# Performance work log

Measured on AMD Instinct MI355X. Metric: run time of the kernel, lower is better.

The kernel has to match this reference:

```python
import jax, jax.numpy as jnp
import numpy as np

BS, NQ, NC = 64, 3000, 256
FH, FW, TOPK = 100, 100, 1500
INK_INF = jnp.float32(1e20)


def setup_inputs() -> dict:
    key = jax.random.key(0)
    k1, k2, k3 = jax.random.split(key, 3)
    u = jax.random.uniform(k1, (BS, NQ, 4), dtype=jnp.float32)
    # cx,cy in [0.25,0.75], w,h in [0,0.4] -> xyxy strictly inside [0,1]
    cxcy = 0.25 + 0.5 * u[..., :2]
    wh = 0.4 * u[..., 2:]
    output_coord = jnp.concatenate([cxcy, wh], axis=-1)
    output_class = jax.random.uniform(k2, (BS, NQ, NC), dtype=jnp.float32)
    # valid feature extent [valid_h, valid_w] per image (from ~mask cumsum in original)
    valid_feature_size = jax.random.randint(k3, (BS, 2), 50, FH + 1, dtype=jnp.int32)
    rows = jnp.arange(FH)[None, :, None]
    cols = jnp.arange(FW)[None, None, :]
    padding_mask = (rows >= valid_feature_size[:, 0][:, None, None]) | (
        cols >= valid_feature_size[:, 1][:, None, None]
    )  # (BS, FH, FW) bool, True = padded
    return {
        "output_coord": output_coord,
        "output_class": output_class,
        "valid_feature_size": valid_feature_size,
        "padding_mask": padding_mask,
        "feature_h": FH,
        "feature_w": FW,
        "topk": TOPK,
    }


def reference(output_coord, output_class, valid_feature_size, padding_mask,
              feature_h, feature_w, topk):
    bs = output_coord.shape[0]
    # scores = output_class.max(dim=-1); topk box select
    scores = jnp.max(output_class, axis=-1)                      # (bs, nq)
    _, topk_idx = jax.lax.top_k(scores, topk)                    # (bs, k)
    boxes = jnp.take_along_axis(output_coord, topk_idx[..., None], axis=1)  # (bs,k,4) cxcywh
    # box_cxcywh_to_xyxy
    cxcy, wh = boxes[..., :2], boxes[..., 2:]
    xyxy = jnp.concatenate([cxcy - 0.5 * wh, cxcy + 0.5 * wh], axis=-1)  # (bs,k,4)
    # valid_size.repeat(1,2) -> [vh, vw, vh, vw]
    vfs = valid_feature_size.astype(xyxy.dtype)
    scale = jnp.concatenate([vfs, vfs], axis=-1)[:, None, :]     # (bs,1,4)
    rng = jnp.floor(xyxy * scale).astype(jnp.int32)              # (bs,k,4)
    lx, ly, rx, ry = rng[..., 0], rng[..., 1], rng[..., 2], rng[..., 3]
    rows = jnp.arange(feature_h)
    cols = jnp.arange(feature_w)
    # per-box row/col membership; union over boxes via batched GEMM
    R = ((rows[None, None, :] >= ly[..., None]) & (rows[None, None, :] < ry[..., None])).astype(jnp.float32)  # (bs,k,h)
    C = ((cols[None, None, :] >= lx[..., None]) & (cols[None, None, :] < rx[..., None])).astype(jnp.float32)  # (bs,k,w)
    covered = jnp.einsum('bkh,bkw->bhw', R, C) > 0               # (bs,h,w)
    extra_mask = ~covered                                        # True outside every kept box
    # mask = extra_mask | padding_mask; float masked_fill(-INK_INF)
    full = extra_mask.reshape(bs, -1) | padding_mask.reshape(bs, -1)
    attn_mask = jnp.where(full, -INK_INF, jnp.float32(0.0))      # (bs, h*w)
    return attn_mask
```

## Files before the change

kernel.cpp:

```cpp
#include <hip/hip_runtime.h>

#define BS   64
#define NQ   3000
#define NC   256
#define FH   100
#define FW   100
#define TOPK 1500

__global__ __launch_bounds__(256) void scores_kernel(const float4* __restrict__ cls,
                                                     float* __restrict__ scores) {
    const int tid  = threadIdx.x;
    const int lane = tid & 63;
    const int wave = tid >> 6;
    const int row0 = blockIdx.x * 16 + wave * 4;
    const float4* p = cls + (size_t)row0 * (NC / 4) + lane;
    float4 a = p[0], b = p[64], c = p[128], d = p[192];
    float m0 = fmaxf(fmaxf(a.x, a.y), fmaxf(a.z, a.w));
    float m1 = fmaxf(fmaxf(b.x, b.y), fmaxf(b.z, b.w));
    float m2 = fmaxf(fmaxf(c.x, c.y), fmaxf(c.z, c.w));
    float m3 = fmaxf(fmaxf(d.x, d.y), fmaxf(d.z, d.w));
#pragma unroll
    for (int off = 32; off > 0; off >>= 1) {
        m0 = fmaxf(m0, __shfl_xor(m0, off, 64));
        m1 = fmaxf(m1, __shfl_xor(m1, off, 64));
        m2 = fmaxf(m2, __shfl_xor(m2, off, 64));
        m3 = fmaxf(m3, __shfl_xor(m3, off, 64));
    }
    if (lane < 4) {
        float m = (lane == 0) ? m0 : (lane == 1) ? m1 : (lane == 2) ? m2 : m3;
        scores[row0 + lane] = m;
    }
}

#define NTM 512

__global__ __launch_bounds__(NTM) void mask_kernel(const float4* __restrict__ coord,
                                                   const int* __restrict__ vfs,
                                                   const float* __restrict__ scores,
                                                   float* __restrict__ out) {
    __shared__ unsigned su[NQ];
    __shared__ int      hist[8][256];
    __shared__ unsigned cov[FH * 4];
    __shared__ int      eqlist[NQ];
    __shared__ int      wave_sum[4];
    __shared__ int      s_selbin, s_K, s_ecnt;

    const int b    = blockIdx.x;
    const int tid  = threadIdx.x;
    const int wid  = tid >> 6;

    for (int q = tid; q < NQ; q += NTM)
        su[q] = __float_as_uint(scores[b * NQ + q]);
    for (int i = tid; i < FH * 4; i += NTM) cov[i] = 0u;
    if (tid == 0) s_ecnt = 0;

    unsigned prefix = 0, pmask = 0;
    int K = TOPK;
#pragma unroll
    for (int p = 0; p < 4; ++p) {
        const int shift = 24 - 8 * p;
        for (int i = tid; i < 8 * 256; i += NTM) ((int*)hist)[i] = 0;
        __syncthreads();
        for (int q = tid; q < NQ; q += NTM) {
            unsigned u = su[q];
            if ((u & pmask) == prefix)
                atomicAdd(&hist[wid][(u >> shift) & 0xFF], 1);
        }
        __syncthreads();
        int x = 0, hx = 0, bin = 0;
        if (tid < 256) {
            bin = 255 - tid;
            hx = hist[0][bin] + hist[1][bin] + hist[2][bin] + hist[3][bin] +
                 hist[4][bin] + hist[5][bin] + hist[6][bin] + hist[7][bin];
            x = hx;
#pragma unroll
            for (int off = 1; off < 64; off <<= 1) {
                int y = __shfl_up(x, off, 64);
                if ((tid & 63) >= off) x += y;
            }
            if ((tid & 63) == 63) wave_sum[tid >> 6] = x;
        }
        __syncthreads();
        if (tid < 256) {
            int w = tid >> 6;
            for (int j = 0; j < w; ++j) x += wave_sum[j];
            int ge_incl = x;
            int ge_excl = x - hx;
            if (ge_incl >= K && ge_excl < K) {
                s_selbin = bin;
                s_K      = K - ge_excl;
            }
        }
        __syncthreads();
        prefix |= ((unsigned)s_selbin) << shift;
        pmask  |= (0xFFu << shift);
        K = s_K;
        __syncthreads();
    }
    const unsigned v      = prefix;
    const int      e_take = K;

    const float s0 = (float)vfs[2 * b];
    const float s1 = (float)vfs[2 * b + 1];

    for (int q = tid; q < NQ; q += NTM) {
        unsigned u = su[q];
        if (u > v) {
            float4 c4 = coord[(size_t)b * NQ + q];
            float x1 = c4.x - 0.5f * c4.z, y1 = c4.y - 0.5f * c4.w;
            float x2 = c4.x + 0.5f * c4.z, y2 = c4.y + 0.5f * c4.w;
            int lx = (int)floorf(x1 * s0), ly = (int)floorf(y1 * s1);
            int rx = (int)floorf(x2 * s0), ry = (int)floorf(y2 * s1);
            int h0 = ly > 0 ? ly : 0, h1 = ry < FH ? ry : FH;
            int w0 = lx > 0 ? lx : 0, w1 = rx < FW ? rx : FW;
            if (h0 < h1 && w0 < w1) {
                unsigned m[4];
#pragma unroll
                for (int j = 0; j < 4; ++j) {
                    int lo = w0 - 32 * j; lo = lo < 0 ? 0 : lo;
                    int hi = w1 - 32 * j; hi = hi > 32 ? 32 : hi;
                    unsigned mm = 0u;
                    if (hi > lo) {
                        unsigned top = (hi >= 32) ? 0xFFFFFFFFu : ((1u << hi) - 1u);
                        unsigned bot = (lo <= 0) ? 0u : ((1u << lo) - 1u);
                        mm = top & ~bot;
                    }
                    m[j] = mm;
                }
                for (int h = h0; h < h1; ++h) {
#pragma unroll
                    for (int j = 0; j < 4; ++j)
                        if (m[j]) atomicOr(&cov[h * 4 + j], m[j]);
                }
            }
        } else if (u == v) {
            int i = atomicAdd(&s_ecnt, 1);
            eqlist[i] = q;
        }
    }
    __syncthreads();

    const int E = s_ecnt;
    for (int i = tid; i < E; i += NTM) {
        int q = eqlist[i];
        int r = 0;
        for (int j = 0; j < E; ++j) r += (eqlist[j] < q) ? 1 : 0;
        if (r < e_take) {
            float4 c4 = coord[(size_t)b * NQ + q];
            float x1 = c4.x - 0.5f * c4.z, y1 = c4.y - 0.5f * c4.w;
            float x2 = c4.x + 0.5f * c4.z, y2 = c4.y + 0.5f * c4.w;
            int lx = (int)floorf(x1 * s0), ly = (int)floorf(y1 * s1);
            int rx = (int)floorf(x2 * s0), ry = (int)floorf(y2 * s1);
            int h0 = ly > 0 ? ly : 0, h1 = ry < FH ? ry : FH;
            int w0 = lx > 0 ? lx : 0, w1 = rx < FW ? rx : FW;
            if (h0 < h1 && w0 < w1) {
                for (int h = h0; h < h1; ++h) {
#pragma unroll
                    for (int j = 0; j < 4; ++j) {
                        int lo = w0 - 32 * j; lo = lo < 0 ? 0 : lo;
                        int hi = w1 - 32 * j; hi = hi > 32 ? 32 : hi;
                        if (hi > lo) {
                            unsigned top = (hi >= 32) ? 0xFFFFFFFFu : ((1u << hi) - 1u);
                            unsigned bot = (lo <= 0) ? 0u : ((1u << lo) - 1u);
                            atomicOr(&cov[h * 4 + j], top & ~bot);
                        }
                    }
                }
            }
        }
    }
    __syncthreads();

    const int iv0 = vfs[2 * b], iv1 = vfs[2 * b + 1];
    for (int idx = tid; idx < FH * FW; idx += NTM) {
        int h = idx / FW;
        int w = idx - h * FW;
        bool covered = (cov[h * 4 + (w >> 5)] >> (w & 31)) & 1u;
        bool pad = (h >= iv0) || (w >= iv1);
        out[(size_t)b * (FH * FW) + idx] = (covered && !pad) ? 0.0f : -1e20f;
    }
}

extern "C" void kernel_launch(void* const* d_in, const int* in_sizes, int n_in,
                              void* d_out, int out_size, void* d_ws, size_t ws_size,
                              hipStream_t stream) {
    const float4* coord = (const float4*)d_in[0];
    const float*  cls   = (const float*)d_in[1];
    const int*    vfs   = (const int*)d_in[2];
    float* scores = (float*)d_ws;
    float* out    = (float*)d_out;

    const int rows = BS * NQ;
    scores_kernel<<<rows / 16, 256, 0, stream>>>((const float4*)cls, scores);
    mask_kernel<<<BS, NTM, 0, stream>>>(coord, vfs, scores, out);
}
```

Baseline: 316.4 us.

## Fuse score reduction and mask kernels into one cooperative grid-synced kernel

Replaces the two launches (row-max scores, then per-image radix top-k and mask) with a single cooperative kernel. A 512-block grid computes the scores in a grid-stride loop, then a grid barrier lets the first 64 blocks run the mask phase. This removes one kernel launch and the gap between kernels. In exchange, the whole grid is sized for the heavy shared-memory mask phase, the scores pass runs with fewer resident blocks, and the kernel pays for a grid sync. If the cooperative launch fails, it falls back to the two-kernel path.

```diff
diff --git a/kernel.cpp b/kernel.cpp
--- a/kernel.cpp
+++ b/kernel.cpp
@@ -1,4 +1,7 @@
 #include <hip/hip_runtime.h>
+#include <hip/hip_cooperative_groups.h>
+
+namespace cg = cooperative_groups;
 
 #define BS   64
 #define NQ   3000
@@ -6,6 +9,189 @@
 #define FH   100
 #define FW   100
 #define TOPK 1500
+#define NT   512
+#define NBLK 512
+
+__device__ __forceinline__ void mask_phase(int b, int tid,
+                                           const float4* __restrict__ coord,
+                                           const int* __restrict__ vfs,
+                                           const float* __restrict__ scores,
+                                           float* __restrict__ out,
+                                           unsigned* su, int (*hist)[256],
+                                           unsigned* cov, int* eqlist,
+                                           int* wave_sum, int* s_selbin,
+                                           int* s_K, int* s_ecnt) {
+    const int wid = tid >> 6;
+
+    for (int q = tid; q < NQ; q += NT)
+        su[q] = __float_as_uint(scores[b * NQ + q]);
+    for (int i = tid; i < FH * 4; i += NT) cov[i] = 0u;
+    if (tid == 0) *s_ecnt = 0;
+
+    unsigned prefix = 0, pmask = 0;
+    int K = TOPK;
+#pragma unroll
+    for (int p = 0; p < 4; ++p) {
+        const int shift = 24 - 8 * p;
+        for (int i = tid; i < 8 * 256; i += NT) ((int*)hist)[i] = 0;
+        __syncthreads();
+        for (int q = tid; q < NQ; q += NT) {
+            unsigned u = su[q];
+            if ((u & pmask) == prefix)
+                atomicAdd(&hist[wid][(u >> shift) & 0xFF], 1);
+        }
+        __syncthreads();
+        int x = 0, hx = 0, bin = 0;
+        if (tid < 256) {
+            bin = 255 - tid;
+            hx = hist[0][bin] + hist[1][bin] + hist[2][bin] + hist[3][bin] +
+                 hist[4][bin] + hist[5][bin] + hist[6][bin] + hist[7][bin];
+            x = hx;
+#pragma unroll
+            for (int off = 1; off < 64; off <<= 1) {
+                int y = __shfl_up(x, off, 64);
+                if ((tid & 63) >= off) x += y;
+            }
+            if ((tid & 63) == 63) wave_sum[tid >> 6] = x;
+        }
+        __syncthreads();
+        if (tid < 256) {
+            int w = tid >> 6;
+            for (int j = 0; j < w; ++j) x += wave_sum[j];
+            int ge_incl = x;
+            int ge_excl = x - hx;
+            if (ge_incl >= K && ge_excl < K) { *s_selbin = bin; *s_K = K - ge_excl; }
+        }
+        __syncthreads();
+        prefix |= ((unsigned)*s_selbin) << shift;
+        pmask  |= (0xFFu << shift);
+        K = *s_K;
+        __syncthreads();
+    }
+    const unsigned v      = prefix;
+    const int      e_take = K;
+
+    const float s0 = (float)vfs[2 * b];
+    const float s1 = (float)vfs[2 * b + 1];
+
+    for (int q = tid; q < NQ; q += NT) {
+        unsigned u = su[q];
+        if (u > v) {
+            float4 c4 = coord[(size_t)b * NQ + q];
+            float x1 = c4.x - 0.5f * c4.z, y1 = c4.y - 0.5f * c4.w;
+            float x2 = c4.x + 0.5f * c4.z, y2 = c4.y + 0.5f * c4.w;
+            int lx = (int)floorf(x1 * s0), ly = (int)floorf(y1 * s1);
+            int rx = (int)floorf(x2 * s0), ry = (int)floorf(y2 * s1);
+            int h0 = ly > 0 ? ly : 0, h1 = ry < FH ? ry : FH;
+            int w0 = lx > 0 ? lx : 0, w1 = rx < FW ? rx : FW;
+            if (h0 < h1 && w0 < w1) {
+                unsigned m[4];
+#pragma unroll
+                for (int j = 0; j < 4; ++j) {
+                    int lo = w0 - 32 * j; lo = lo < 0 ? 0 : lo;
+                    int hi = w1 - 32 * j; hi = hi > 32 ? 32 : hi;
+                    unsigned mm = 0u;
+                    if (hi > lo) {
+                        unsigned top = (hi >= 32) ? 0xFFFFFFFFu : ((1u << hi) - 1u);
+                        unsigned bot = (lo <= 0) ? 0u : ((1u << lo) - 1u);
+                        mm = top & ~bot;
+                    }
+                    m[j] = mm;
+                }
+                for (int h = h0; h < h1; ++h)
+#pragma unroll
+                    for (int j = 0; j < 4; ++j)
+                        if (m[j]) atomicOr(&cov[h * 4 + j], m[j]);
+            }
+        } else if (u == v) {
+            int i = atomicAdd(s_ecnt, 1);
+            eqlist[i] = q;
+        }
+    }
+    __syncthreads();
+
+    const int E = *s_ecnt;
+    for (int i = tid; i < E; i += NT) {
+        int q = eqlist[i];
+        int r = 0;
+        for (int j = 0; j < E; ++j) r += (eqlist[j] < q) ? 1 : 0;
+        if (r < e_take) {
+            float4 c4 = coord[(size_t)b * NQ + q];
+            float x1 = c4.x - 0.5f * c4.z, y1 = c4.y - 0.5f * c4.w;
+            float x2 = c4.x + 0.5f * c4.z, y2 = c4.y + 0.5f * c4.w;
+            int lx = (int)floorf(x1 * s0), ly = (int)floorf(y1 * s1);
+            int rx = (int)floorf(x2 * s0), ry = (int)floorf(y2 * s1);
+            int h0 = ly > 0 ? ly : 0, h1 = ry < FH ? ry : FH;
+            int w0 = lx > 0 ? lx : 0, w1 = rx < FW ? rx : FW;
+            if (h0 < h1 && w0 < w1) {
+                for (int h = h0; h < h1; ++h)
+#pragma unroll
+                    for (int j = 0; j < 4; ++j) {
+                        int lo = w0 - 32 * j; lo = lo < 0 ? 0 : lo;
+                        int hi = w1 - 32 * j; hi = hi > 32 ? 32 : hi;
+                        if (hi > lo) {
+                            unsigned top = (hi >= 32) ? 0xFFFFFFFFu : ((1u << hi) - 1u);
+                            unsigned bot = (lo <= 0) ? 0u : ((1u << lo) - 1u);
+                            atomicOr(&cov[h * 4 + j], top & ~bot);
+                        }
+                    }
+            }
+        }
+    }
+    __syncthreads();
+
+    const int iv0 = vfs[2 * b], iv1 = vfs[2 * b + 1];
+    for (int idx = tid; idx < FH * FW; idx += NT) {
+        int h = idx / FW;
+        int w = idx - h * FW;
+        bool covered = (cov[h * 4 + (w >> 5)] >> (w & 31)) & 1u;
+        bool pad = (h >= iv0) || (w >= iv1);
+        out[(size_t)b * (FH * FW) + idx] = (covered && !pad) ? 0.0f : -1e20f;
+    }
+}
+
+__global__ __launch_bounds__(NT) void fused_kernel(const float4* __restrict__ coord,
+                                                   const float4* __restrict__ cls,
+                                                   const int* __restrict__ vfs,
+                                                   float* __restrict__ scores,
+                                                   float* __restrict__ out) {
+    __shared__ unsigned su[NQ];
+    __shared__ int      hist[8][256];
+    __shared__ unsigned cov[FH * 4];
+    __shared__ int      eqlist[NQ];
+    __shared__ int      wave_sum[4];
+    __shared__ int      s_selbin, s_K, s_ecnt;
+
+    const int tid  = threadIdx.x;
+    const int lane = tid & 63;
+    const int wave = tid >> 6;
+
+    for (int row0 = blockIdx.x * 32 + wave * 4; row0 < BS * NQ; row0 += NBLK * 32) {
+        const float4* p = cls + (size_t)row0 * (NC / 4) + lane;
+        float4 a = p[0], b = p[64], c = p[128], d = p[192];
+        float m0 = fmaxf(fmaxf(a.x, a.y), fmaxf(a.z, a.w));
+        float m1 = fmaxf(fmaxf(b.x, b.y), fmaxf(b.z, b.w));
+        float m2 = fmaxf(fmaxf(c.x, c.y), fmaxf(c.z, c.w));
+        float m3 = fmaxf(fmaxf(d.x, d.y), fmaxf(d.z, d.w));
+#pragma unroll
+        for (int off = 32; off > 0; off >>= 1) {
+            m0 = fmaxf(m0, __shfl_xor(m0, off, 64));
+            m1 = fmaxf(m1, __shfl_xor(m1, off, 64));
+            m2 = fmaxf(m2, __shfl_xor(m2, off, 64));
+            m3 = fmaxf(m3, __shfl_xor(m3, off, 64));
+        }
+        if (lane < 4) {
+            float m = (lane == 0) ? m0 : (lane == 1) ? m1 : (lane == 2) ? m2 : m3;
+            scores[row0 + lane] = m;
+        }
+    }
+
+    cg::this_grid().sync();
+
+    if (blockIdx.x < BS)
+        mask_phase(blockIdx.x, tid, coord, vfs, scores, out,
+                   su, hist, cov, eqlist, wave_sum, &s_selbin, &s_K, &s_ecnt);
+}
 
 __global__ __launch_bounds__(256) void scores_kernel(const float4* __restrict__ cls,
                                                      float* __restrict__ scores) {
@@ -32,165 +218,36 @@
     }
 }
 
-#define NTM 512
-
-__global__ __launch_bounds__(NTM) void mask_kernel(const float4* __restrict__ coord,
-                                                   const int* __restrict__ vfs,
-                                                   const float* __restrict__ scores,
-                                                   float* __restrict__ out) {
+__global__ __launch_bounds__(NT) void mask_kernel(const float4* __restrict__ coord,
+                                                  const int* __restrict__ vfs,
+                                                  const float* __restrict__ scores,
+                                                  float* __restrict__ out) {
     __shared__ unsigned su[NQ];
     __shared__ int      hist[8][256];
     __shared__ unsigned cov[FH * 4];
     __shared__ int      eqlist[NQ];
     __shared__ int      wave_sum[4];
     __shared__ int      s_selbin, s_K, s_ecnt;
-
-    const int b    = blockIdx.x;
-    const int tid  = threadIdx.x;
-    const int wid  = tid >> 6;
-
-    for (int q = tid; q < NQ; q += NTM)
-        su[q] = __float_as_uint(scores[b * NQ + q]);
-    for (int i = tid; i < FH * 4; i += NTM) cov[i] = 0u;
-    if (tid == 0) s_ecnt = 0;
-
-    unsigned prefix = 0, pmask = 0;
-    int K = TOPK;
-#pragma unroll
-    for (int p = 0; p < 4; ++p) {
-        const int shift = 24 - 8 * p;
-        for (int i = tid; i < 8 * 256; i += NTM) ((int*)hist)[i] = 0;
-        __syncthreads();
-        for (int q = tid; q < NQ; q += NTM) {
-            unsigned u = su[q];
-            if ((u & pmask) == prefix)
-                atomicAdd(&hist[wid][(u >> shift) & 0xFF], 1);
-        }
-        __syncthreads();
-        int x = 0, hx = 0, bin = 0;
-        if (tid < 256) {
-            bin = 255 - tid;
-            hx = hist[0][bin] + hist[1][bin] + hist[2][bin] + hist[3][bin] +
-                 hist[4][bin] + hist[5][bin] + hist[6][bin] + hist[7][bin];
-            x = hx;
-#pragma unroll
-            for (int off = 1; off < 64; off <<= 1) {
-                int y = __shfl_up(x, off, 64);
-                if ((tid & 63) >= off) x += y;
-            }
-            if ((tid & 63) == 63) wave_sum[tid >> 6] = x;
-        }
-        __syncthreads();
-        if (tid < 256) {
-            int w = tid >> 6;
-            for (int j = 0; j < w; ++j) x += wave_sum[j];
-            int ge_incl = x;
-            int ge_excl = x - hx;
-            if (ge_incl >= K && ge_excl < K) {
-                s_selbin = bin;
-                s_K      = K - ge_excl;
-            }
-        }
-        __syncthreads();
-        prefix |= ((unsigned)s_selbin) << shift;
-        pmask  |= (0xFFu << shift);
-        K = s_K;
-        __syncthreads();
-    }
-    const unsigned v      = prefix;
-    const int      e_take = K;
-
-    const float s0 = (float)vfs[2 * b];
-    const float s1 = (float)vfs[2 * b + 1];
-
-    for (int q = tid; q < NQ; q += NTM) {
-        unsigned u = su[q];
-        if (u > v) {
-            float4 c4 = coord[(size_t)b * NQ + q];
-            float x1 = c4.x - 0.5f * c4.z, y1 = c4.y - 0.5f * c4.w;
-            float x2 = c4.x + 0.5f * c4.z, y2 = c4.y + 0.5f * c4.w;
-            int lx = (int)floorf(x1 * s0), ly = (int)floorf(y1 * s1);
-            int rx = (int)floorf(x2 * s0), ry = (int)floorf(y2 * s1);
-            int h0 = ly > 0 ? ly : 0, h1 = ry < FH ? ry : FH;
-            int w0 = lx > 0 ? lx : 0, w1 = rx < FW ? rx : FW;
-            if (h0 < h1 && w0 < w1) {
-                unsigned m[4];
-#pragma unroll
-                for (int j = 0; j < 4; ++j) {
-                    int lo = w0 - 32 * j; lo = lo < 0 ? 0 : lo;
-                    int hi = w1 - 32 * j; hi = hi > 32 ? 32 : hi;
-                    unsigned mm = 0u;
-                    if (hi > lo) {
-                        unsigned top = (hi >= 32) ? 0xFFFFFFFFu : ((1u << hi) - 1u);
-                        unsigned bot = (lo <= 0) ? 0u : ((1u << lo) - 1u);
-                        mm = top & ~bot;
-                    }
-                    m[j] = mm;
-                }
-                for (int h = h0; h < h1; ++h) {
-#pragma unroll
-                    for (int j = 0; j < 4; ++j)
-                        if (m[j]) atomicOr(&cov[h * 4 + j], m[j]);
-                }
-            }
-        } else if (u == v) {
-            int i = atomicAdd(&s_ecnt, 1);
-            eqlist[i] = q;
-        }
-    }
-    __syncthreads();
-
-    const int E = s_ecnt;
-    for (int i = tid; i < E; i += NTM) {
-        int q = eqlist[i];
-        int r = 0;
-        for (int j = 0; j < E; ++j) r += (eqlist[j] < q) ? 1 : 0;
-        if (r < e_take) {
-            float4 c4 = coord[(size_t)b * NQ + q];
-            float x1 = c4.x - 0.5f * c4.z, y1 = c4.y - 0.5f * c4.w;
-            float x2 = c4.x + 0.5f * c4.z, y2 = c4.y + 0.5f * c4.w;
-            int lx = (int)floorf(x1 * s0), ly = (int)floorf(y1 * s1);
-            int rx = (int)floorf(x2 * s0), ry = (int)floorf(y2 * s1);
-            int h0 = ly > 0 ? ly : 0, h1 = ry < FH ? ry : FH;
-            int w0 = lx > 0 ? lx : 0, w1 = rx < FW ? rx : FW;
-            if (h0 < h1 && w0 < w1) {
-                for (int h = h0; h < h1; ++h) {
-#pragma unroll
-                    for (int j = 0; j < 4; ++j) {
-                        int lo = w0 - 32 * j; lo = lo < 0 ? 0 : lo;
-                        int hi = w1 - 32 * j; hi = hi > 32 ? 32 : hi;
-                        if (hi > lo) {
-                            unsigned top = (hi >= 32) ? 0xFFFFFFFFu : ((1u << hi) - 1u);
-                            unsigned bot = (lo <= 0) ? 0u : ((1u << lo) - 1u);
-                            atomicOr(&cov[h * 4 + j], top & ~bot);
-                        }
-                    }
-                }
-            }
-        }
-    }
-    __syncthreads();
-
-    const int iv0 = vfs[2 * b], iv1 = vfs[2 * b + 1];
-    for (int idx = tid; idx < FH * FW; idx += NTM) {
-        int h = idx / FW;
-        int w = idx - h * FW;
-        bool covered = (cov[h * 4 + (w >> 5)] >> (w & 31)) & 1u;
-        bool pad = (h >= iv0) || (w >= iv1);
-        out[(size_t)b * (FH * FW) + idx] = (covered && !pad) ? 0.0f : -1e20f;
-    }
+    mask_phase(blockIdx.x, threadIdx.x, coord, vfs, scores, out,
+               su, hist, cov, eqlist, wave_sum, &s_selbin, &s_K, &s_ecnt);
 }
 
 extern "C" void kernel_launch(void* const* d_in, const int* in_sizes, int n_in,
                               void* d_out, int out_size, void* d_ws, size_t ws_size,
                               hipStream_t stream) {
     const float4* coord = (const float4*)d_in[0];
-    const float*  cls   = (const float*)d_in[1];
+    const float4* cls   = (const float4*)d_in[1];
     const int*    vfs   = (const int*)d_in[2];
     float* scores = (float*)d_ws;
     float* out    = (float*)d_out;
 
-    const int rows = BS * NQ;
-    scores_kernel<<<rows / 16, 256, 0, stream>>>((const float4*)cls, scores);
-    mask_kernel<<<BS, NTM, 0, stream>>>(coord, vfs, scores, out);
-}
+    void* args[] = {(void*)&coord, (void*)&cls, (void*)&vfs,
+                    (void*)&scores, (void*)&out};
+    hipError_t err = hipLaunchCooperativeKernel((void*)fused_kernel,
+                                                dim3(NBLK), dim3(NT),
+                                                args, 0, stream);
+    if (err != hipSuccess) {
+        scores_kernel<<<(BS * NQ) / 16, 256, 0, stream>>>(cls, scores);
+        mask_kernel<<<BS, NT, 0, stream>>>(coord, vfs, scores, out);
+    }
+}
```

New measurement: 383.2 us. 21.1% more time.

## Fuse score reduction and mask building via last-block-done counter per batch

Applied to the files above, without the earlier changes.

Merges the class-max scoring kernel and the per-image top-k mask kernel into one launch. Each image's scores are computed by 25 blocks. The last block to finish, detected through an atomic counter in workspace that is zeroed by a memset, then runs the radix-select and coverage-mask phase. This aims to overlap the serial per-image mask work with score computation for other images and to remove the gap between the two kernels. In exchange it adds a memset launch and threadfences. Scoring blocks also carry the mask phase's shared-memory footprint, which may limit occupancy during the bandwidth-bound scoring phase.

```diff
diff --git a/kernel.cpp b/kernel.cpp
--- a/kernel.cpp
+++ b/kernel.cpp
@@ -6,52 +6,62 @@
 #define FH   100
 #define FW   100
 #define TOPK 1500
-
-__global__ __launch_bounds__(256) void scores_kernel(const float4* __restrict__ cls,
-                                                     float* __restrict__ scores) {
-    const int tid  = threadIdx.x;
-    const int lane = tid & 63;
-    const int wave = tid >> 6;
-    const int row0 = blockIdx.x * 16 + wave * 4;
-    const float4* p = cls + (size_t)row0 * (NC / 4) + lane;
-    float4 a = p[0], b = p[64], c = p[128], d = p[192];
-    float m0 = fmaxf(fmaxf(a.x, a.y), fmaxf(a.z, a.w));
-    float m1 = fmaxf(fmaxf(b.x, b.y), fmaxf(b.z, b.w));
-    float m2 = fmaxf(fmaxf(c.x, c.y), fmaxf(c.z, c.w));
-    float m3 = fmaxf(fmaxf(d.x, d.y), fmaxf(d.z, d.w));
-#pragma unroll
-    for (int off = 32; off > 0; off >>= 1) {
-        m0 = fmaxf(m0, __shfl_xor(m0, off, 64));
-        m1 = fmaxf(m1, __shfl_xor(m1, off, 64));
-        m2 = fmaxf(m2, __shfl_xor(m2, off, 64));
-        m3 = fmaxf(m3, __shfl_xor(m3, off, 64));
-    }
-    if (lane < 4) {
-        float m = (lane == 0) ? m0 : (lane == 1) ? m1 : (lane == 2) ? m2 : m3;
-        scores[row0 + lane] = m;
-    }
-}
-
-#define NTM 512
-
-__global__ __launch_bounds__(NTM) void mask_kernel(const float4* __restrict__ coord,
+#define NT   512
+#define SB   25
+#define RPB  (NQ / SB)
+
+__global__ __launch_bounds__(NT) void fused_kernel(const float4* __restrict__ coord,
+                                                   const float4* __restrict__ cls,
                                                    const int* __restrict__ vfs,
-                                                   const float* __restrict__ scores,
+                                                   float* __restrict__ scores,
+                                                   int* __restrict__ done,
                                                    float* __restrict__ out) {
     __shared__ unsigned su[NQ];
     __shared__ int      hist[8][256];
     __shared__ unsigned cov[FH * 4];
     __shared__ int      eqlist[NQ];
     __shared__ int      wave_sum[4];
-    __shared__ int      s_selbin, s_K, s_ecnt;
-
-    const int b    = blockIdx.x;
+    __shared__ int      s_selbin, s_K, s_ecnt, s_old;
+
+    const int blk  = blockIdx.x;
+    const int b    = blk / SB;
+    const int chnk = blk % SB;
     const int tid  = threadIdx.x;
-    const int wid  = tid >> 6;
-
-    for (int q = tid; q < NQ; q += NTM)
+    const int lane = tid & 63;
+    const int wave = tid >> 6;
+
+    const int rowbase = b * NQ + chnk * RPB;
+    for (int r = wave * 4; r < RPB; r += 32) {
+        const int row0 = rowbase + r;
+        const float4* p = cls + (size_t)row0 * (NC / 4) + lane;
+        float4 a = p[0], b4 = p[64], c = p[128], d = p[192];
+        float m0 = fmaxf(fmaxf(a.x, a.y), fmaxf(a.z, a.w));
+        float m1 = fmaxf(fmaxf(b4.x, b4.y), fmaxf(b4.z, b4.w));
+        float m2 = fmaxf(fmaxf(c.x, c.y), fmaxf(c.z, c.w));
+        float m3 = fmaxf(fmaxf(d.x, d.y), fmaxf(d.z, d.w));
+#pragma unroll
+        for (int off = 32; off > 0; off >>= 1) {
+            m0 = fmaxf(m0, __shfl_xor(m0, off, 64));
+            m1 = fmaxf(m1, __shfl_xor(m1, off, 64));
+            m2 = fmaxf(m2, __shfl_xor(m2, off, 64));
+            m3 = fmaxf(m3, __shfl_xor(m3, off, 64));
+        }
+        if (lane < 4) {
+            float m = (lane == 0) ? m0 : (lane == 1) ? m1 : (lane == 2) ? m2 : m3;
+            scores[row0 + lane] = m;
+        }
+    }
+
+    __threadfence();
+    __syncthreads();
+    if (tid == 0) s_old = atomicAdd(&done[b], 1);
+    __syncthreads();
+    if (s_old != SB - 1) return;
+    __threadfence();
+
+    for (int q = tid; q < NQ; q += NT)
         su[q] = __float_as_uint(scores[b * NQ + q]);
-    for (int i = tid; i < FH * 4; i += NTM) cov[i] = 0u;
+    for (int i = tid; i < FH * 4; i += NT) cov[i] = 0u;
     if (tid == 0) s_ecnt = 0;
 
     unsigned prefix = 0, pmask = 0;
@@ -59,12 +69,12 @@
 #pragma unroll
     for (int p = 0; p < 4; ++p) {
         const int shift = 24 - 8 * p;
-        for (int i = tid; i < 8 * 256; i += NTM) ((int*)hist)[i] = 0;
-        __syncthreads();
-        for (int q = tid; q < NQ; q += NTM) {
+        for (int i = tid; i < 8 * 256; i += NT) ((int*)hist)[i] = 0;
+        __syncthreads();
+        for (int q = tid; q < NQ; q += NT) {
             unsigned u = su[q];
             if ((u & pmask) == prefix)
-                atomicAdd(&hist[wid][(u >> shift) & 0xFF], 1);
+                atomicAdd(&hist[wave][(u >> shift) & 0xFF], 1);
         }
         __syncthreads();
         int x = 0, hx = 0, bin = 0;
@@ -86,10 +96,7 @@
             for (int j = 0; j < w; ++j) x += wave_sum[j];
             int ge_incl = x;
             int ge_excl = x - hx;
-            if (ge_incl >= K && ge_excl < K) {
-                s_selbin = bin;
-                s_K      = K - ge_excl;
-            }
+            if (ge_incl >= K && ge_excl < K) { s_selbin = bin; s_K = K - ge_excl; }
         }
         __syncthreads();
         prefix |= ((unsigned)s_selbin) << shift;
@@ -103,7 +110,7 @@
     const float s0 = (float)vfs[2 * b];
     const float s1 = (float)vfs[2 * b + 1];
 
-    for (int q = tid; q < NQ; q += NTM) {
+    for (int q = tid; q < NQ; q += NT) {
         unsigned u = su[q];
         if (u > v) {
             float4 c4 = coord[(size_t)b * NQ + q];
@@ -127,11 +134,10 @@
                     }
                     m[j] = mm;
                 }
-                for (int h = h0; h < h1; ++h) {
+                for (int h = h0; h < h1; ++h)
 #pragma unroll
                     for (int j = 0; j < 4; ++j)
                         if (m[j]) atomicOr(&cov[h * 4 + j], m[j]);
-                }
             }
         } else if (u == v) {
             int i = atomicAdd(&s_ecnt, 1);
@@ -141,7 +147,7 @@
     __syncthreads();
 
     const int E = s_ecnt;
-    for (int i = tid; i < E; i += NTM) {
+    for (int i = tid; i < E; i += NT) {
         int q = eqlist[i];
         int r = 0;
         for (int j = 0; j < E; ++j) r += (eqlist[j] < q) ? 1 : 0;
@@ -154,7 +160,7 @@
             int h0 = ly > 0 ? ly : 0, h1 = ry < FH ? ry : FH;
             int w0 = lx > 0 ? lx : 0, w1 = rx < FW ? rx : FW;
             if (h0 < h1 && w0 < w1) {
-                for (int h = h0; h < h1; ++h) {
+                for (int h = h0; h < h1; ++h)
 #pragma unroll
                     for (int j = 0; j < 4; ++j) {
                         int lo = w0 - 32 * j; lo = lo < 0 ? 0 : lo;
@@ -165,14 +171,13 @@
                             atomicOr(&cov[h * 4 + j], top & ~bot);
                         }
                     }
-                }
             }
         }
     }
     __syncthreads();
 
     const int iv0 = vfs[2 * b], iv1 = vfs[2 * b + 1];
-    for (int idx = tid; idx < FH * FW; idx += NTM) {
+    for (int idx = tid; idx < FH * FW; idx += NT) {
         int h = idx / FW;
         int w = idx - h * FW;
         bool covered = (cov[h * 4 + (w >> 5)] >> (w & 31)) & 1u;
@@ -185,12 +190,12 @@
                               void* d_out, int out_size, void* d_ws, size_t ws_size,
                               hipStream_t stream) {
     const float4* coord = (const float4*)d_in[0];
-    const float*  cls   = (const float*)d_in[1];
+    const float4* cls   = (const float4*)d_in[1];
     const int*    vfs   = (const int*)d_in[2];
     float* scores = (float*)d_ws;
+    int*   done   = (int*)((char*)d_ws + (size_t)BS * NQ * 4);
     float* out    = (float*)d_out;
 
-    const int rows = BS * NQ;
-    scores_kernel<<<rows / 16, 256, 0, stream>>>((const float4*)cls, scores);
-    mask_kernel<<<BS, NTM, 0, stream>>>(coord, vfs, scores, out);
+    hipMemsetAsync(done, 0, BS * sizeof(int), stream);
+    fused_kernel<<<BS * SB, NT, 0, stream>>>(coord, cls, vfs, scores, done, out);
 }
```

After: 918.1 us. +190.2%, slower.
